# Kernel tuning notes

Hardware: AMD Instinct MI355X
Metric: run time of the kernel (lower is better)

## Reference

```python
import jax, jax.numpy as jnp
import numpy as np

DIM = 1024
HEADS = 16
HEAD_DIM = DIM // HEADS
SCALE = HEAD_DIM ** -0.5


def setup_inputs() -> dict:
    key = jax.random.key(0)
    k1, k2, k3, k4 = jax.random.split(key, 4)
    x = jax.random.normal(k1, (8, 1024, DIM), dtype=jnp.float32)
    # qkv: Linear(dim, 3*dim), bias=False; proj: Linear(dim, dim) with bias
    w_qkv = jax.random.normal(k2, (DIM, 3 * DIM), dtype=jnp.float32) * (DIM ** -0.5)
    w_proj = jax.random.normal(k3, (DIM, DIM), dtype=jnp.float32) * (DIM ** -0.5)
    b_proj = jax.random.normal(k4, (DIM,), dtype=jnp.float32) * 0.02
    return {"x": x, "w_qkv": w_qkv, "w_proj": w_proj, "b_proj": b_proj}


def reference(x, w_qkv, w_proj, b_proj):
    b, n, dim = x.shape
    h, d = HEADS, HEAD_DIM
    qkv = x @ w_qkv                                  # [b, n, 3*dim]
    qkv = qkv.reshape(b, n, 3, h, d)                  # split (qkv h d)
    q = jnp.transpose(qkv[:, :, 0], (0, 2, 1, 3))     # [b, h, n, d]
    k = jnp.transpose(qkv[:, :, 1], (0, 2, 1, 3))
    v = jnp.transpose(qkv[:, :, 2], (0, 2, 1, 3))
    dots = jnp.einsum('bhid,bhjd->bhij', q, k) * SCALE
    attn = jax.nn.softmax(dots, axis=-1)              # [b, h, n, n]
    out = jnp.einsum('bhij,bhjd->bhid', attn, v)      # [b, h, n, d]
    out = jnp.transpose(out, (0, 2, 1, 3)).reshape(b, n, dim)
    return out @ w_proj + b_proj
```

## Files before the change

kernel.cpp:

```cpp
#include <hip/hip_runtime.h>
#include <hip/hip_bf16.h>
#include <stdint.h>


typedef __attribute__((ext_vector_type(8))) short  short8;
typedef __attribute__((ext_vector_type(4))) float  floatx4;

#define MFMA_BF16(a, b, c) __builtin_amdgcn_mfma_f32_16x16x32_bf16((a), (b), (c), 0, 0, 0)

__device__ __forceinline__ uint16_t f2b(float f) {
    uint32_t i; __builtin_memcpy(&i, &f, 4);
    uint32_t r = i + 0x7FFFu + ((i >> 16) & 1u);
    return (uint16_t)(r >> 16);
}

__device__ __forceinline__ void async16(uint16_t* lds, const uint16_t* g) {
    __builtin_amdgcn_global_load_lds(
        (const __attribute__((address_space(1))) uint32_t*)g,
        (__attribute__((address_space(3))) uint32_t*)lds,
        16, 0, 0);
}

__global__ __launch_bounds__(256) void cvt_f32_bf16(
    const float* __restrict__ in, uint16_t* __restrict__ out, int n4)
{
    const int i = blockIdx.x * 256 + threadIdx.x;
    if (i < n4) {
        const float4 v = ((const float4*)in)[i];
        ushort4 o;
        o.x = f2b(v.x); o.y = f2b(v.y); o.z = f2b(v.z); o.w = f2b(v.w);
        ((ushort4*)out)[i] = o;
    }
}

__global__ __launch_bounds__(256) void transpose_k(
    const float* __restrict__ in, uint16_t* __restrict__ out, int R, int C)
{
    __shared__ uint16_t t[32][33];
    const int bx = blockIdx.x * 32;
    const int by = blockIdx.y * 32;
    const int tx = threadIdx.x & 31, ty = threadIdx.x >> 5;
    #pragma unroll
    for (int j = 0; j < 32; j += 8)
        t[ty + j][tx] = f2b(in[(size_t)(by + ty + j) * C + bx + tx]);
    __syncthreads();
    #pragma unroll
    for (int j = 0; j < 32; j += 8)
        out[(size_t)(bx + ty + j) * R + by + tx] = t[tx][ty + j];
}

template <int EPI>
__global__ __launch_bounds__(256, 2) void gemm_bt(
    const uint16_t* __restrict__ A, const uint16_t* __restrict__ Bt,
    uint16_t* __restrict__ C, float* __restrict__ Cf,
    const float* __restrict__ bias, int M, int N, int K)
{
    __shared__ uint16_t As[128 * 64];
    __shared__ uint16_t Bs[128 * 64];

    const int tid  = threadIdx.x;
    const int lane = tid & 63, quad = lane >> 4, l16 = lane & 15;
    const int wv   = tid >> 6;
    const int wm   = (wv >> 1) * 64, wn = (wv & 1) * 64;

    const int lid = blockIdx.y * gridDim.x + blockIdx.x;
    const int nxl = gridDim.x >> 3;
    const int xcd = lid & 7, loc = lid >> 3;
    const int bx  = xcd * nxl + (loc % nxl);
    const int by  = loc / nxl;
    const int tm  = by * 128, tn = bx * 128;

    floatx4 acc[4][4] = {};

    for (int kt = 0; kt < K; kt += 64) {
        __syncthreads();
        #pragma unroll
        for (int i = 0; i < 4; i++) {
            const int li  = i * 256 + tid;
            const int row = li >> 3;
            const int cg  = (li & 7) ^ (row & 7);
            async16(&As[li * 8], &A[(size_t)(tm + row) * K + kt + cg * 8]);
        }
        #pragma unroll
        for (int i = 0; i < 4; i++) {
            const int li  = i * 256 + tid;
            const int row = li >> 3;
            const int cg  = (li & 7) ^ (row & 7);
            async16(&Bs[li * 8], &Bt[(size_t)(tn + row) * K + kt + cg * 8]);
        }
        __syncthreads();
        #pragma unroll
        for (int kc = 0; kc < 2; kc++) {
            short8 af[4], bf[4];
            #pragma unroll
            for (int mb = 0; mb < 4; mb++) {
                const int row = wm + mb * 16 + l16;
                const int g   = kc * 4 + quad;
                af[mb] = *(const short8*)&As[row * 64 + ((g ^ (row & 7)) * 8)];
            }
            #pragma unroll
            for (int nb = 0; nb < 4; nb++) {
                const int row = wn + nb * 16 + l16;
                const int g   = kc * 4 + quad;
                bf[nb] = *(const short8*)&Bs[row * 64 + ((g ^ (row & 7)) * 8)];
            }
            #pragma unroll
            for (int mb = 0; mb < 4; mb++)
                #pragma unroll
                for (int nb = 0; nb < 4; nb++)
                    acc[mb][nb] = MFMA_BF16(af[mb], bf[nb], acc[mb][nb]);
        }
    }

    if (EPI == 0) {
        const int which = (tn + wn) >> 10;
        if (which == 2) {
            #pragma unroll
            for (int nb = 0; nb < 4; nb++) {
                const int col = tn + wn + nb * 16 + l16;
                const int hh = (col >> 6) & 15, dd = col & 63;
                #pragma unroll
                for (int mb = 0; mb < 4; mb++) {
                    const int gm = tm + wm + mb * 16 + quad * 4;
                    const int b  = gm >> 10, n = gm & 1023;
                    const size_t rgn = (size_t)(256 + b * 16 + hh) * 65536;
                    ushort4 o;
                    o.x = f2b(acc[mb][nb][0]); o.y = f2b(acc[mb][nb][1]);
                    o.z = f2b(acc[mb][nb][2]); o.w = f2b(acc[mb][nb][3]);
                    *(ushort4*)&C[rgn + (size_t)dd * 1024 + n] = o;
                }
            }
        } else {
            #pragma unroll
            for (int nb = 0; nb < 4; nb++) {
                const int col = tn + wn + nb * 16 + l16;
                const int hh = (col >> 6) & 15, dd = col & 63;
                #pragma unroll
                for (int mb = 0; mb < 4; mb++)
                    #pragma unroll
                    for (int r = 0; r < 4; r++) {
                        const int gm = tm + wm + mb * 16 + quad * 4 + r;
                        const int b  = gm >> 10, n = gm & 1023;
                        const size_t rgn = (size_t)(which * 128 + b * 16 + hh) * 65536;
                        C[rgn + (size_t)n * 64 + dd] = f2b(acc[mb][nb][r]);
                    }
            }
        }
    } else {
        #pragma unroll
        for (int nb = 0; nb < 4; nb++) {
            const int col = tn + wn + nb * 16 + l16;
            const float bv = bias[col];
            #pragma unroll
            for (int mb = 0; mb < 4; mb++)
                #pragma unroll
                for (int r = 0; r < 4; r++) {
                    const int gm = tm + wm + mb * 16 + quad * 4 + r;
                    Cf[(size_t)gm * N + col] = acc[mb][nb][r] + bv;
                }
        }
    }
}

__global__ __launch_bounds__(256, 3) void attn_fa(
    const uint16_t* __restrict__ qkv, uint16_t* __restrict__ out)
{
    __shared__ uint16_t Ks[128 * 64];
    __shared__ uint16_t Vs[64 * 128];
    __shared__ uint16_t Ps[4][32 * 72];

    const int tid  = threadIdx.x;
    const int lane = tid & 63, quad = lane >> 4, l16 = lane & 15;
    const int wv   = tid >> 6;
    const int bh   = blockIdx.y;
    const int q0   = blockIdx.x * 128 + wv * 32;

    const size_t qbase  = (size_t)bh * 65536;
    const size_t kbase  = (size_t)(128 + bh) * 65536;
    const size_t vtbase = (size_t)(256 + bh) * 65536;

    short8 qf[2][2];
    #pragma unroll
    for (int qb = 0; qb < 2; qb++)
        #pragma unroll
        for (int ks = 0; ks < 2; ks++)
            qf[qb][ks] = *(const short8*)&qkv[qbase + (size_t)(q0 + qb * 16 + l16) * 64 + ks * 32 + quad * 8];

    floatx4 Oacc[2][4] = {};
    float lpart[2][4] = {};

    constexpr float EXPSCALE = 0.1803368801111244f;

    for (int kb = 0; kb < 8; kb++) {
        __syncthreads();
        #pragma unroll
        for (int i = 0; i < 4; i++) {
            const int li  = i * 256 + tid;
            const int row = li >> 3;
            const int cg  = (li & 7) ^ (row & 7);
            async16(&Ks[li * 8], &qkv[kbase + (size_t)(kb * 128 + row) * 64 + cg * 8]);
        }
        #pragma unroll
        for (int i = 0; i < 4; i++) {
            const int li  = i * 256 + tid;
            const int row = li >> 4;
            const int cg  = (li & 15) ^ (row & 15);
            async16(&Vs[li * 8], &qkv[vtbase + (size_t)row * 1024 + kb * 128 + cg * 8]);
        }
        __syncthreads();

        #pragma unroll
        for (int h = 0; h < 2; h++) {
            floatx4 s[2][4];
            #pragma unroll
            for (int cb = 0; cb < 4; cb++) {
                const int krow = h * 64 + cb * 16 + l16;
                short8 kf0, kf1;
                {
                    const int g0 = quad, g1 = 4 + quad;
                    kf0 = *(const short8*)&Ks[krow * 64 + ((g0 ^ (krow & 7)) * 8)];
                    kf1 = *(const short8*)&Ks[krow * 64 + ((g1 ^ (krow & 7)) * 8)];
                }
                #pragma unroll
                for (int qb = 0; qb < 2; qb++) {
                    floatx4 z = {};
                    z = MFMA_BF16(qf[qb][0], kf0, z);
                    z = MFMA_BF16(qf[qb][1], kf1, z);
                    s[qb][cb] = z;
                }
            }
            #pragma unroll
            for (int qb = 0; qb < 2; qb++)
                #pragma unroll
                for (int cb = 0; cb < 4; cb++)
                    #pragma unroll
                    for (int r = 0; r < 4; r++) {
                        const float p = exp2f(s[qb][cb][r] * EXPSCALE);
                        s[qb][cb][r] = p;
                        lpart[qb][r] += p;
                    }
            #pragma unroll
            for (int qb = 0; qb < 2; qb++)
                #pragma unroll
                for (int cb = 0; cb < 4; cb++)
                    #pragma unroll
                    for (int r = 0; r < 4; r++)
                        Ps[wv][(qb * 16 + quad * 4 + r) * 72 + cb * 16 + l16] =
                            f2b(s[qb][cb][r]);

            short8 pf[2][2];
            #pragma unroll
            for (int qb = 0; qb < 2; qb++)
                #pragma unroll
                for (int kk = 0; kk < 2; kk++)
                    pf[qb][kk] = *(const short8*)&Ps[wv][(qb * 16 + l16) * 72 + kk * 32 + quad * 8];

            #pragma unroll
            for (int nb = 0; nb < 4; nb++) {
                #pragma unroll
                for (int kk = 0; kk < 2; kk++) {
                    const int vrow = nb * 16 + l16;
                    const int g    = h * 8 + kk * 4 + quad;
                    short8 vf = *(const short8*)&Vs[vrow * 128 + ((g ^ (vrow & 15)) * 8)];
                    #pragma unroll
                    for (int qb = 0; qb < 2; qb++)
                        Oacc[qb][nb] = MFMA_BF16(pf[qb][kk], vf, Oacc[qb][nb]);
                }
            }
        }
    }

    #pragma unroll
    for (int qb = 0; qb < 2; qb++)
        #pragma unroll
        for (int r = 0; r < 4; r++) {
            float l = lpart[qb][r];
            #pragma unroll
            for (int off = 1; off < 16; off <<= 1) l += __shfl_xor(l, off);
            lpart[qb][r] = 1.f / l;
        }

    const int b = bh >> 4, hh = bh & 15;
    #pragma unroll
    for (int qb = 0; qb < 2; qb++)
        #pragma unroll
        for (int nb = 0; nb < 4; nb++)
            #pragma unroll
            for (int r = 0; r < 4; r++) {
                const int n = q0 + qb * 16 + quad * 4 + r;
                out[((size_t)(b * 1024 + n)) * 1024 + hh * 64 + nb * 16 + l16] =
                    f2b(Oacc[qb][nb][r] * lpart[qb][r]);
            }
}

extern "C" void kernel_launch(void* const* d_in, const int* in_sizes, int n_in,
                              void* d_out, int out_size, void* d_ws, size_t ws_size,
                              hipStream_t stream)
{
    const float* x      = (const float*)d_in[0];
    const float* w_qkv  = (const float*)d_in[1];
    const float* w_proj = (const float*)d_in[2];
    const float* b_proj = (const float*)d_in[3];
    float* out = (float*)d_out;

    uint16_t* ws   = (uint16_t*)d_ws;
    uint16_t* xb   = ws;
    uint16_t* wTq  = xb  + 8192 * 1024;
    uint16_t* wTp  = wTq + 3072 * 1024;
    uint16_t* qkvb = wTp + 1024 * 1024;
    uint16_t* ao   = xb;

    cvt_f32_bf16<<<8192, 256, 0, stream>>>(x, xb, 8192 * 1024 / 4);
    transpose_k<<<dim3(96, 32), 256, 0, stream>>>(w_qkv, wTq, 1024, 3072);
    transpose_k<<<dim3(32, 32), 256, 0, stream>>>(w_proj, wTp, 1024, 1024);
    gemm_bt<0><<<dim3(24, 64), 256, 0, stream>>>(xb, wTq, qkvb, nullptr, nullptr, 8192, 3072, 1024);
    attn_fa<<<dim3(8, 128), 256, 0, stream>>>(qkvb, ao);
    gemm_bt<1><<<dim3(8, 64), 256, 0, stream>>>(ao, wTp, nullptr, out, b_proj, 8192, 1024, 1024);
}
```

Before: 263.5 us.

## Compute transposed scores, fold softmax scale into Q, pack bf16 stores

The QKV GEMM epilogue now multiplies Q by the scale times log2(e), so the attention kernel can call exp2 without a per-element multiply. Scores are computed as K·Q^T, which leaves each lane holding one query column. The row-sum then stays in a per-lane scalar and needs only two cross-lane shuffles instead of a 4-step reduction per row. P is written to LDS as packed 64-bit bf16 stores, and a hardware packed bf16 convert is used when the builtin exists. This cuts ALU, shuffle and LDS store instruction counts, at the cost of rounding Q to bf16 after scaling, which slightly changes numerics.

```diff
diff --git a/kernel.cpp b/kernel.cpp
--- a/kernel.cpp
+++ b/kernel.cpp
@@ -12,6 +12,22 @@
     uint32_t i; __builtin_memcpy(&i, &f, 4);
     uint32_t r = i + 0x7FFFu + ((i >> 16) & 1u);
     return (uint16_t)(r >> 16);
+}
+
+#if defined(__has_builtin)
+#if __has_builtin(__builtin_amdgcn_cvt_pk_bf16_f32)
+#define HAVE_PK_BF16 1
+#endif
+#endif
+
+__device__ __forceinline__ uint32_t pk_bf16(float a, float b) {
+#ifdef HAVE_PK_BF16
+    typedef __attribute__((ext_vector_type(2))) __bf16 bf16x2;
+    bf16x2 v = __builtin_amdgcn_cvt_pk_bf16_f32(a, b);
+    uint32_t u; __builtin_memcpy(&u, &v, 4); return u;
+#else
+    return (uint32_t)f2b(a) | ((uint32_t)f2b(b) << 16);
+#endif
 }
 
 __device__ __forceinline__ void async16(uint16_t* lds, const uint16_t* g) {
@@ -124,13 +140,14 @@
                     const int gm = tm + wm + mb * 16 + quad * 4;
                     const int b  = gm >> 10, n = gm & 1023;
                     const size_t rgn = (size_t)(256 + b * 16 + hh) * 65536;
-                    ushort4 o;
-                    o.x = f2b(acc[mb][nb][0]); o.y = f2b(acc[mb][nb][1]);
-                    o.z = f2b(acc[mb][nb][2]); o.w = f2b(acc[mb][nb][3]);
-                    *(ushort4*)&C[rgn + (size_t)dd * 1024 + n] = o;
+                    uint2 o;
+                    o.x = pk_bf16(acc[mb][nb][0], acc[mb][nb][1]);
+                    o.y = pk_bf16(acc[mb][nb][2], acc[mb][nb][3]);
+                    *(uint2*)&C[rgn + (size_t)dd * 1024 + n] = o;
                 }
             }
         } else {
+            const float qs = (which == 0) ? 0.18033688011112043f : 1.0f;
             #pragma unroll
             for (int nb = 0; nb < 4; nb++) {
                 const int col = tn + wn + nb * 16 + l16;
@@ -142,7 +159,7 @@
                         const int gm = tm + wm + mb * 16 + quad * 4 + r;
                         const int b  = gm >> 10, n = gm & 1023;
                         const size_t rgn = (size_t)(which * 128 + b * 16 + hh) * 65536;
-                        C[rgn + (size_t)n * 64 + dd] = f2b(acc[mb][nb][r]);
+                        C[rgn + (size_t)n * 64 + dd] = f2b(acc[mb][nb][r] * qs);
                     }
             }
         }
@@ -181,15 +198,13 @@
 
     short8 qf[2][2];
     #pragma unroll
-    for (int qb = 0; qb < 2; qb++)
+    for (int nq = 0; nq < 2; nq++)
         #pragma unroll
         for (int ks = 0; ks < 2; ks++)
-            qf[qb][ks] = *(const short8*)&qkv[qbase + (size_t)(q0 + qb * 16 + l16) * 64 + ks * 32 + quad * 8];
+            qf[nq][ks] = *(const short8*)&qkv[qbase + (size_t)(q0 + nq * 16 + l16) * 64 + ks * 32 + quad * 8];
 
     floatx4 Oacc[2][4] = {};
-    float lpart[2][4] = {};
-
-    constexpr float EXPSCALE = 0.1803368801111244f;
+    float lpart[2] = {0.f, 0.f};
 
     for (int kb = 0; kb < 8; kb++) {
         __syncthreads();
@@ -211,52 +226,48 @@
 
         #pragma unroll
         for (int h = 0; h < 2; h++) {
-            floatx4 s[2][4];
-            #pragma unroll
-            for (int cb = 0; cb < 4; cb++) {
-                const int krow = h * 64 + cb * 16 + l16;
-                short8 kf0, kf1;
-                {
-                    const int g0 = quad, g1 = 4 + quad;
-                    kf0 = *(const short8*)&Ks[krow * 64 + ((g0 ^ (krow & 7)) * 8)];
-                    kf1 = *(const short8*)&Ks[krow * 64 + ((g1 ^ (krow & 7)) * 8)];
-                }
-                #pragma unroll
-                for (int qb = 0; qb < 2; qb++) {
+            floatx4 st[4][2];
+            #pragma unroll
+            for (int mb = 0; mb < 4; mb++) {
+                const int krow = h * 64 + mb * 16 + l16;
+                const int g0 = quad, g1 = 4 + quad;
+                short8 kf0 = *(const short8*)&Ks[krow * 64 + ((g0 ^ (krow & 7)) * 8)];
+                short8 kf1 = *(const short8*)&Ks[krow * 64 + ((g1 ^ (krow & 7)) * 8)];
+                #pragma unroll
+                for (int nq = 0; nq < 2; nq++) {
                     floatx4 z = {};
-                    z = MFMA_BF16(qf[qb][0], kf0, z);
-                    z = MFMA_BF16(qf[qb][1], kf1, z);
-                    s[qb][cb] = z;
-                }
-            }
-            #pragma unroll
-            for (int qb = 0; qb < 2; qb++)
-                #pragma unroll
-                for (int cb = 0; cb < 4; cb++)
+                    z = MFMA_BF16(kf0, qf[nq][0], z);
+                    z = MFMA_BF16(kf1, qf[nq][1], z);
+                    st[mb][nq] = z;
+                }
+            }
+            #pragma unroll
+            for (int mb = 0; mb < 4; mb++)
+                #pragma unroll
+                for (int nq = 0; nq < 2; nq++)
                     #pragma unroll
                     for (int r = 0; r < 4; r++) {
-                        const float p = exp2f(s[qb][cb][r] * EXPSCALE);
-                        s[qb][cb][r] = p;
-                        lpart[qb][r] += p;
+                        const float p = exp2f(st[mb][nq][r]);
+                        st[mb][nq][r] = p;
+                        lpart[nq] += p;
                     }
             #pragma unroll
-            for (int qb = 0; qb < 2; qb++)
-                #pragma unroll
-                for (int cb = 0; cb < 4; cb++)
-                    #pragma unroll
-                    for (int r = 0; r < 4; r++)
-                        Ps[wv][(qb * 16 + quad * 4 + r) * 72 + cb * 16 + l16] =
-                            f2b(s[qb][cb][r]);
-
+            for (int nq = 0; nq < 2; nq++)
+                #pragma unroll
+                for (int mb = 0; mb < 4; mb++) {
+                    uint2 w;
+                    w.x = pk_bf16(st[mb][nq][0], st[mb][nq][1]);
+                    w.y = pk_bf16(st[mb][nq][2], st[mb][nq][3]);
+                    *(uint2*)&Ps[wv][(nq * 16 + l16) * 72 + mb * 16 + quad * 4] = w;
+                }
             short8 pf[2][2];
             #pragma unroll
             for (int qb = 0; qb < 2; qb++)
                 #pragma unroll
                 for (int kk = 0; kk < 2; kk++)
                     pf[qb][kk] = *(const short8*)&Ps[wv][(qb * 16 + l16) * 72 + kk * 32 + quad * 8];
-
-            #pragma unroll
-            for (int nb = 0; nb < 4; nb++) {
+            #pragma unroll
+            for (int nb = 0; nb < 4; nb++)
                 #pragma unroll
                 for (int kk = 0; kk < 2; kk++) {
                     const int vrow = nb * 16 + l16;
@@ -266,19 +277,23 @@
                     for (int qb = 0; qb < 2; qb++)
                         Oacc[qb][nb] = MFMA_BF16(pf[qb][kk], vf, Oacc[qb][nb]);
                 }
-            }
-        }
-    }
-
+        }
+    }
+
+    float linv[2];
+    #pragma unroll
+    for (int nq = 0; nq < 2; nq++) {
+        float l = lpart[nq];
+        l += __shfl_xor(l, 16);
+        l += __shfl_xor(l, 32);
+        linv[nq] = 1.f / l;
+    }
+    float inv[2][4];
     #pragma unroll
     for (int qb = 0; qb < 2; qb++)
         #pragma unroll
-        for (int r = 0; r < 4; r++) {
-            float l = lpart[qb][r];
-            #pragma unroll
-            for (int off = 1; off < 16; off <<= 1) l += __shfl_xor(l, off);
-            lpart[qb][r] = 1.f / l;
-        }
+        for (int r = 0; r < 4; r++)
+            inv[qb][r] = __shfl(linv[qb], quad * 4 + r);
 
     const int b = bh >> 4, hh = bh & 15;
     #pragma unroll
@@ -289,7 +304,7 @@
             for (int r = 0; r < 4; r++) {
                 const int n = q0 + qb * 16 + quad * 4 + r;
                 out[((size_t)(b * 1024 + n)) * 1024 + hh * 64 + nb * 16 + l16] =
-                    f2b(Oacc[qb][nb][r] * lpart[qb][r]);
+                    f2b(Oacc[qb][nb][r] * inv[qb][r]);
             }
 }
 
```

New measurement: 243.9 us. 7.4% less time.
